# Optimization experiments

Hardware: AMD Instinct MI355X
Metric: run time of the kernel (lower is better)

Reference implementation:

```python
import jax, jax.numpy as jnp
import numpy as np

B, S, D, H, HD = 2, 4096, 768, 12, 64
W = 256          # one-sided window (attention_window=512)
G = 128          # number of global tokens (prefix)
NB = S // W      # sequence blocks
EPS = 1e-5


def _heads(x, w, b):
    # [B,S,D] -> [B,H,S,HD]
    return (x @ w + b).reshape(B, S, H, HD).transpose(0, 2, 1, 3)


def _blocks(xp):
    # xp: [B,H,S+2W,HD] (padded by W on both sides) -> [B,H,NB,3W,HD]
    # block n holds keys/values at absolute positions [n*W - W, n*W + 2W)
    return jnp.concatenate(
        [xp[:, :, j * W:j * W + S].reshape(B, H, NB, W, HD) for j in range(3)], axis=3)


def setup_inputs() -> dict:
    key = jax.random.key(0)
    ks = jax.random.split(key, 12)
    p = lambda i, shape: jax.random.normal(ks[i], shape, jnp.float32) * 0.02
    z = lambda n: jnp.zeros((n,), jnp.float32)
    return {
        'hidden_states': jax.random.normal(ks[0], (B, S, D), jnp.float32),
        'attention_mask': jnp.zeros((B, S), jnp.float32),  # 0 = local attention, no padding
        'is_index_global_attn': jnp.broadcast_to(jnp.arange(S) < G, (B, S)),
        'Wq': p(1, (D, D)), 'bq': z(D),
        'Wk': p(2, (D, D)), 'bk': z(D),
        'Wv': p(3, (D, D)), 'bv': z(D),
        'Wqg': p(4, (D, D)), 'bqg': z(D),
        'Wkg': p(5, (D, D)), 'bkg': z(D),
        'Wvg': p(6, (D, D)), 'bvg': z(D),
        'Wo': p(7, (D, D)), 'bo': z(D),
        'ln_gamma': jnp.ones((D,), jnp.float32),
        'ln_beta': jnp.zeros((D,), jnp.float32),
    }


def reference(hidden_states, attention_mask, is_index_global_attn,
              Wq, bq, Wk, bk, Wv, bv, Wqg, bqg, Wkg, bkg, Wvg, bvg,
              Wo, bo, ln_gamma, ln_beta):
    scale = 1.0 / np.sqrt(HD)
    q = _heads(hidden_states, Wq, bq) * scale   # [B,H,S,HD]
    k = _heads(hidden_states, Wk, bk)
    v = _heads(hidden_states, Wv, bv)

    pad = ((0, 0), (0, 0), (W, W), (0, 0))
    kb = _blocks(jnp.pad(k, pad))                # [B,H,NB,3W,HD]
    vb = _blocks(jnp.pad(v, pad))
    qb = q.reshape(B, H, NB, W, HD)
    s_band = jnp.einsum('bhnqd,bhnkd->bhnqk', qb, kb)   # [B,H,NB,W,3W]

    # band + boundary mask; global keys are removed from windowed attention
    # (they appear as dedicated prepended columns instead, as in HF Longformer)
    qi = jnp.arange(W)[:, None]                  # query offset in block
    kk = jnp.arange(3 * W)[None, :]              # key offset in 3W window
    rel = kk - W - qi                            # [W,3W] relative position
    kpos = jnp.arange(NB)[:, None, None] * W + (kk - W)[None]  # [NB,W(1),3W] absolute key pos
    valid = (jnp.abs(rel) <= W)[None] & (kpos >= G) & (kpos < S)  # [NB,W,3W]
    s_band = jnp.where(valid[None, None], s_band, -1e9)

    # global key columns (regular k/v projections, per HF Longformer)
    kg, vg = k[:, :, :G], v[:, :, :G]
    s_glob = jnp.einsum('bhsd,bhgd->bhsg', q, kg)        # [B,H,S,G]
    scores = jnp.concatenate([s_glob, s_band.reshape(B, H, S, 3 * W)], axis=-1)
    probs = jax.nn.softmax(scores, axis=-1)
    p_glob = probs[..., :G]
    p_band = probs[..., G:].reshape(B, H, NB, W, 3 * W)
    out = (jnp.einsum('bhnqk,bhnkd->bhnqd', p_band, vb).reshape(B, H, S, HD)
           + jnp.einsum('bhsg,bhgd->bhsd', p_glob, vg))

    # global query tokens attend to everything via the *_global projections;
    # their outputs overwrite the windowed outputs (HF behavior)
    qg = _heads(hidden_states, Wqg, bqg)[:, :, :G] * scale
    kgf = _heads(hidden_states, Wkg, bkg)
    vgf = _heads(hidden_states, Wvg, bvg)
    pg = jax.nn.softmax(jnp.einsum('bhgd,bhsd->bhgs', qg, kgf), axis=-1)
    og = jnp.einsum('bhgs,bhsd->bhgd', pg, vgf)
    out = out.at[:, :, :G].set(og)

    # TFLongformerSelfOutput: dense + residual + LayerNorm
    ctx = out.transpose(0, 2, 1, 3).reshape(B, S, D)
    y = ctx @ Wo + bo + hidden_states
    mu = y.mean(-1, keepdims=True)
    var = ((y - mu) ** 2).mean(-1, keepdims=True)
    return (y - mu) / jnp.sqrt(var + EPS) * ln_gamma + ln_beta
```

## Files before the change

kernel.cpp:

```cpp
#include <hip/hip_runtime.h>
#include <stdint.h>

#define BB 2
#define SS 4096
#define DD 768
#define HH 12
#define HDD 64
#define WW 256
#define GG 128
#define NBB 16
#define NSPLIT 16

typedef __attribute__((ext_vector_type(4))) float f32x4;
typedef __attribute__((ext_vector_type(16))) float f32x16;
typedef __attribute__((ext_vector_type(8))) short bf16x8;
typedef __attribute__((ext_vector_type(4))) short s16x4;
typedef __attribute__((ext_vector_type(4))) unsigned short u16x4;

__device__ __forceinline__ unsigned short f2bf(float x) {
  union { float f; unsigned int u; } v; v.f = x;
  return (unsigned short)((v.u + 0x7fffu + ((v.u >> 16) & 1u)) >> 16);
}

__device__ __forceinline__ void async16(void* lds, const void* g) {
  __builtin_amdgcn_global_load_lds(
      (const __attribute__((address_space(1))) unsigned int*)g,
      (__attribute__((address_space(3))) unsigned int*)lds, 16, 0, 0);
}

__device__ __forceinline__ uint32_t lds_b(const void* p) {
  return (uint32_t)(uintptr_t)(__attribute__((address_space(3))) const void*)p;
}

__device__ __forceinline__ s16x4 tr_read(uint32_t addr) {
  s16x4 d;
  asm volatile("ds_read_b64_tr_b16 %0, %1" : "=v"(d) : "v"(addr) : "memory");
  return d;
}

__device__ __forceinline__ unsigned int cvtpk(float lo, float hi) {
  unsigned int d;
  asm("v_cvt_pk_bf16_f32 %0, %1, %2" : "=v"(d) : "v"(lo), "v"(hi));
  return d;
}

__device__ __forceinline__ void plswap(int& a, int& b) {
  auto r = __builtin_amdgcn_permlane32_swap(a, b, false, false);
  a = r[0]; b = r[1];
}

__device__ __forceinline__ float xhalf(float x, int hi) {
  int a = __float_as_int(x), b = a;
  auto r = __builtin_amdgcn_permlane32_swap(a, b, false, false);
  return __int_as_float(hi ? r[0] : r[1]);
}

__global__ __launch_bounds__(256) void k_cvt(const float* __restrict__ x,
                                             unsigned short* __restrict__ o, int n4) {
  int i = blockIdx.x * 256 + threadIdx.x;
  if (i >= n4) return;
  f32x4 v = ((const f32x4*)x)[i];
  u16x4 r;
  r[0] = f2bf(v[0]); r[1] = f2bf(v[1]); r[2] = f2bf(v[2]); r[3] = f2bf(v[3]);
  ((u16x4*)o)[i] = r;
}

struct WArgs {
  const float* s[7];
  unsigned short* d[7];
};
__global__ __launch_bounds__(256) void k_tw(WArgs a) {
  __shared__ float t[64][65];
  const float* src = a.s[blockIdx.z];
  unsigned short* dst = a.d[blockIdx.z];
  int n0 = blockIdx.x * 64, k0 = blockIdx.y * 64;
#pragma unroll
  for (int it = 0; it < 16; ++it) {
    int idx = it * 256 + threadIdx.x;
    int r = idx >> 6, c = idx & 63;
    t[r][c] = src[(size_t)(k0 + r) * DD + n0 + c];
  }
  __syncthreads();
#pragma unroll
  for (int it = 0; it < 16; ++it) {
    int idx = it * 256 + threadIdx.x;
    int r = idx >> 6, c = idx & 63;
    dst[(size_t)(n0 + r) * DD + k0 + c] = f2bf(t[c][r]);
  }
}

template <int OMODE>
__global__ __launch_bounds__(256) void k_gemm(
    const unsigned short* __restrict__ A, const unsigned short* __restrict__ Wt,
    const float* __restrict__ b0, const float* __restrict__ b1,
    const float* __restrict__ b2, const float* __restrict__ b3,
    const float* __restrict__ b4, unsigned short* __restrict__ outH,
    float* __restrict__ outY, const float* __restrict__ resid) {
  const int bm = blockIdx.x;
  int bn, p;
  if (OMODE == 0) { p = blockIdx.y / 6; bn = blockIdx.y % 6; }
  else { p = 0; bn = blockIdx.y; }
  const float* bias = b0;
  if (OMODE == 0) bias = (p == 0) ? b0 : (p == 1) ? b1 : (p == 2) ? b2 : (p == 3) ? b3 : b4;
  const float scale = (OMODE == 1 || (OMODE == 0 && p == 0)) ? 0.125f : 1.0f;

  __shared__ unsigned short Asm_[128 * 64];
  __shared__ unsigned short Bsm_[128 * 64];
  const int tid = threadIdx.x;
  const int l = tid & 63, w = tid >> 6;
  const int wr = w >> 1, wc = w & 1;
  const int g = l >> 4, ln = l & 15;
  const int l3 = l >> 3, l7 = l & 7;
  const int slotsrc = l7 ^ l3;

  f32x4 zf = {0.f, 0.f, 0.f, 0.f};
  f32x4 acc[4][4];
#pragma unroll
  for (int i = 0; i < 4; ++i)
#pragma unroll
    for (int j = 0; j < 4; ++j) acc[i][j] = zf;

  const int wtrow0 = (OMODE == 0 ? p * DD : 0) + bn * 128;

  for (int kt = 0; kt < 12; ++kt) {
#pragma unroll
    for (int i = 0; i < 4; ++i) {
      int u = i * 4 + w;
      int row = u * 8 + l3;
      int ar = bm * 128 + row;
      if (OMODE == 1) ar = ((ar >> 7) << 12) + (ar & 127);
      async16(&Asm_[u * 512], A + (size_t)ar * DD + kt * 64 + slotsrc * 8);
      async16(&Bsm_[u * 512], Wt + (size_t)(wtrow0 + row) * DD + kt * 64 + slotsrc * 8);
    }
    __syncthreads();
#pragma unroll
    for (int kc = 0; kc < 2; ++kc) {
      bf16x8 af[4], bfr[4];
#pragma unroll
      for (int t = 0; t < 4; ++t) {
        int arow = wr * 64 + t * 16 + ln;
        af[t] = *(const bf16x8*)&Asm_[arow * 64 + (((kc * 4 + g) ^ (arow & 7)) << 3)];
        int brow = wc * 64 + t * 16 + ln;
        bfr[t] = *(const bf16x8*)&Bsm_[brow * 64 + (((kc * 4 + g) ^ (brow & 7)) << 3)];
      }
#pragma unroll
      for (int ti = 0; ti < 4; ++ti)
#pragma unroll
        for (int tj = 0; tj < 4; ++tj)
          acc[ti][tj] = __builtin_amdgcn_mfma_f32_16x16x32_bf16(af[ti], bfr[tj], acc[ti][tj], 0, 0, 0);
    }
    __syncthreads();
  }

#pragma unroll
  for (int tj = 0; tj < 4; ++tj) {
    int nl = bn * 128 + wc * 64 + tj * 16 + ln;
    float bv = bias[nl];
#pragma unroll
    for (int ti = 0; ti < 4; ++ti) {
#pragma unroll
      for (int r = 0; r < 4; ++r) {
        int m = bm * 128 + wr * 64 + ti * 16 + g * 4 + r;
        float val = acc[ti][tj][r] + bv;
        if (OMODE == 2) {
          outY[(size_t)m * DD + nl] = val + resid[(size_t)m * DD + nl];
        } else if (OMODE == 0) {
          val *= scale;
          int b = m >> 12, s = m & 4095, h = nl >> 6, d = nl & 63;
          outH[(size_t)p * (BB * HH * SS * HDD) +
               (((size_t)(b * HH + h) * SS + s) * HDD) + d] = f2bf(val);
        } else {
          val *= scale;
          int b = m >> 7, gi = m & 127, h = nl >> 6, d = nl & 63;
          outH[(((size_t)(b * HH + h) * GG + gi) * HDD) + d] = f2bf(val);
        }
      }
    }
  }
}

template <int MODE>
__global__ __launch_bounds__((MODE == 0) ? 512 : 256, 4) void k_attn(
    const unsigned short* __restrict__ qbuf, const unsigned short* __restrict__ kbuf,
    const unsigned short* __restrict__ vbuf, unsigned short* __restrict__ ctx,
    float* __restrict__ Opart, float* __restrict__ mlp) {
  constexpr int NW = (MODE == 0) ? 8 : 4;
  constexpr int NSTG = (MODE == 0) ? 1 : 2;
  constexpr float L2E = 1.4426950408889634f;

  __shared__ unsigned short Ksm[2][64 * 64];
  __shared__ unsigned short Vsm[2][64 * 64];
  __shared__ __align__(16) float Alds[NW][32];

  const int tid = threadIdx.x;
  const int l = tid & 63, w = tid >> 6;
  const int l31 = l & 31, hi = l >> 5;
  const int l3 = l >> 3, l7 = l & 7;

  int b, h, n, split;
  if (MODE == 0) {
    n = blockIdx.x & 15; h = (blockIdx.x >> 4) % 12; b = blockIdx.x / (16 * 12); split = 0;
  } else {
    split = blockIdx.x & 15; int bhid = blockIdx.x >> 4; h = bhid % 12; b = bhid / 12; n = 0;
  }

  const size_t bh = (size_t)(b * HH + h);
  const unsigned short* qp = qbuf + bh * (size_t)((MODE == 0) ? SS * HDD : GG * HDD);
  const unsigned short* kp = kbuf + bh * (size_t)(SS * HDD);
  const unsigned short* vp = vbuf + bh * (size_t)(SS * HDD);

  int bstart = 0, nch;
  if (MODE == 0) {
    bstart = n * 256 - 256;
    int s0 = bstart < GG ? GG : bstart;
    int e0 = bstart + 768; if (e0 > SS) e0 = SS;
    nch = 2 + ((e0 - s0) >> 6);
    bstart = s0;
  } else {
    nch = 4;
  }
  const int qrow0 = (MODE == 0) ? (n * 256 + w * 32) : (w * 32);

  bf16x8 qf[4];
#pragma unroll
  for (int kd = 0; kd < 4; ++kd)
    qf[kd] = *(const bf16x8*)&qp[(size_t)(qrow0 + l31) * HDD + kd * 16 + hi * 8];

  f32x16 O[2];
#pragma unroll
  for (int dt = 0; dt < 2; ++dt)
#pragma unroll
    for (int r = 0; r < 16; ++r) O[dt][r] = 0.f;
  float m2 = -1e30f, lsum = 0.f;

  const uint32_t vbase = lds_b(Vsm);
  int vwoff[NSTG];
  {
    int key0 = tid >> 3, dc = tid & 7;
#pragma unroll
    for (int u = 0; u < NSTG; ++u) {
      int key = u * 32 + key0;
      vwoff[u] = (((key >> 2) << 8) | ((dc >> 1) << 6) | ((key & 3) << 4) | ((dc & 1) << 3));
    }
  }

#define KB_OF(ci) ((ci) < 2 && MODE == 0 ? (ci) * 64 : (MODE == 0 ? bstart + ((ci) - 2) * 64 : ((split * 4 + (ci)) * 64)))

  bf16x8 vv[NSTG];
  {
    int kb = KB_OF(0);
#pragma unroll
    for (int u = 0; u < NSTG; ++u) {
      async16(&Ksm[0][(u * NW + w) * 512],
              kp + (size_t)(kb + (u * NW + w) * 8 + l3) * HDD + ((l7 ^ l3) << 3));
      vv[u] = *(const bf16x8*)&vp[(size_t)(kb + u * 32 + (tid >> 3)) * HDD + ((tid & 7) << 3)];
    }
  }
  int buf = 0;

  for (int ci = 0; ci < nch; ++ci) {
    const int kbase = KB_OF(ci);
    asm volatile("s_waitcnt vmcnt(0)" ::: "memory");
#pragma unroll
    for (int u = 0; u < NSTG; ++u) *(bf16x8*)&Vsm[buf][vwoff[u]] = vv[u];
    __syncthreads();

    if (ci + 1 < nch) {
      int kb = KB_OF(ci + 1);
#pragma unroll
      for (int u = 0; u < NSTG; ++u) {
        async16(&Ksm[buf ^ 1][(u * NW + w) * 512],
                kp + (size_t)(kb + (u * NW + w) * 8 + l3) * HDD + ((l7 ^ l3) << 3));
        vv[u] = *(const bf16x8*)&vp[(size_t)(kb + u * 32 + (tid >> 3)) * HDD + ((tid & 7) << 3)];
      }
    }

    f32x16 sc[2];
#pragma unroll
    for (int s = 0; s < 2; ++s)
#pragma unroll
      for (int r = 0; r < 16; ++r) sc[s][r] = 0.f;
    __builtin_amdgcn_s_setprio(1);
#pragma unroll
    for (int kd = 0; kd < 4; ++kd) {
#pragma unroll
      for (int s = 0; s < 2; ++s) {
        int row = s * 32 + l31;
        bf16x8 kf = *(const bf16x8*)&Ksm[buf][row * 64 + ((((kd << 1) + hi) ^ (row & 7)) << 3)];
        sc[s] = __builtin_amdgcn_mfma_f32_32x32x16_bf16(kf, qf[kd], sc[s], 0, 0, 0);
      }
    }
    __builtin_amdgcn_s_setprio(0);

    if (MODE == 0 && kbase >= GG) {
      const int base0 = (kbase - (n * 256 - 256)) - (w * 32 + l31);
#pragma unroll
      for (int s = 0; s < 2; ++s)
#pragma unroll
        for (int r = 0; r < 16; ++r) {
          int t = base0 + s * 32 + (r & 3) + 8 * (r >> 2) + 4 * hi;
          if ((unsigned)t > 512u) sc[s][r] = -1e9f;
        }
    }

    float mh = sc[0][0];
#pragma unroll
    for (int s = 0; s < 2; ++s)
#pragma unroll
      for (int r = 0; r < 16; ++r) if (s || r) mh = fmaxf(mh, sc[s][r]);
    mh = fmaxf(mh, xhalf(mh, hi));
    float mnew = fmaxf(m2, mh * L2E);
    float alpha = exp2f(m2 - mnew);
    m2 = mnew;
    float sh = 0.f;
#pragma unroll
    for (int s = 0; s < 2; ++s)
#pragma unroll
      for (int r = 0; r < 16; ++r) {
        float pv = exp2f(__builtin_fmaf(sc[s][r], L2E, -mnew));
        sc[s][r] = pv;
        sh += pv;
      }
    sh += xhalf(sh, hi);
    lsum = lsum * alpha + sh;

    if (l < 32) Alds[w][l] = alpha;
    f32x4 aT[4];
#pragma unroll
    for (int g2 = 0; g2 < 4; ++g2) aT[g2] = *(const f32x4*)&Alds[w][g2 * 8 + hi * 4];
#pragma unroll
    for (int dt = 0; dt < 2; ++dt)
#pragma unroll
      for (int r = 0; r < 16; ++r) O[dt][r] *= aT[r >> 2][r & 3];

    bf16x8 pa[4];
#pragma unroll
    for (int kk = 0; kk < 4; ++kk) {
      const int s = kk >> 1, h8 = (kk & 1) * 8;
      int x0 = (int)cvtpk(sc[s][h8 + 0], sc[s][h8 + 1]);
      int x1 = (int)cvtpk(sc[s][h8 + 2], sc[s][h8 + 3]);
      int y0 = (int)cvtpk(sc[s][h8 + 4], sc[s][h8 + 5]);
      int y1 = (int)cvtpk(sc[s][h8 + 6], sc[s][h8 + 7]);
      plswap(x0, y0); plswap(x1, y1);
      union { int u[4]; bf16x8 v; } pk;
      pk.u[0] = x0; pk.u[1] = x1; pk.u[2] = y0; pk.u[3] = y1;
      pa[kk] = pk.v;
    }

    const uint32_t vb = vbase + (uint32_t)(buf << 13);
#pragma unroll
    for (int dt = 0; dt < 2; ++dt) {
      s16x4 t0[4], t1[4];
#pragma unroll
      for (int kk = 0; kk < 4; ++kk) {
        int kg = kk * 4 + hi * 2;
        int dgrp = dt * 2 + (l31 >> 4);
        uint32_t a = vb + (uint32_t)((kg * 256 + dgrp * 64 + (l31 & 15)) << 1);
        t0[kk] = tr_read(a);
        t1[kk] = tr_read(a + 512);
      }
      asm volatile("s_waitcnt lgkmcnt(0)" ::: "memory");
      __builtin_amdgcn_sched_barrier(0);
      __builtin_amdgcn_s_setprio(1);
#pragma unroll
      for (int kk = 0; kk < 4; ++kk) {
        bf16x8 vf = __builtin_shufflevector(t0[kk], t1[kk], 0, 1, 2, 3, 4, 5, 6, 7);
        O[dt] = __builtin_amdgcn_mfma_f32_32x32x16_bf16(pa[kk], vf, O[dt], 0, 0, 0);
      }
      __builtin_amdgcn_s_setprio(0);
    }

    buf ^= 1;
  }

  if (MODE == 0) {
    if (l < 32) Alds[w][l] = 1.f / lsum;
    f32x4 iT[4];
#pragma unroll
    for (int g2 = 0; g2 < 4; ++g2) iT[g2] = *(const f32x4*)&Alds[w][g2 * 8 + hi * 4];
#pragma unroll
    for (int dt = 0; dt < 2; ++dt)
#pragma unroll
      for (int r = 0; r < 16; ++r) {
        int q = qrow0 + (r & 3) + 8 * (r >> 2) + 4 * hi;
        int d = dt * 32 + l31;
        ctx[((size_t)b * SS + q) * DD + h * HDD + d] = f2bf(O[dt][r] * iT[r >> 2][r & 3]);
      }
  } else {
    size_t pb = (bh * NSPLIT + split) * (size_t)GG;
#pragma unroll
    for (int dt = 0; dt < 2; ++dt)
#pragma unroll
      for (int r = 0; r < 16; ++r) {
        int q = w * 32 + (r & 3) + 8 * (r >> 2) + 4 * hi;
        Opart[(pb + q) * HDD + dt * 32 + l31] = O[dt][r];
      }
    if (l < 32) {
      size_t mb = (pb + w * 32 + l) * 2;
      mlp[mb] = m2;
      mlp[mb + 1] = lsum;
    }
  }
#undef KB_OF
}

__global__ __launch_bounds__(256) void k_red(const float* __restrict__ Opart,
                                             const float* __restrict__ mlp,
                                             unsigned short* __restrict__ ctx) {
  int wid = blockIdx.x * 4 + (threadIdx.x >> 6);
  int d = threadIdx.x & 63;
  int bh = wid >> 7, q = wid & 127;
  int b = bh / HH, h = bh % HH;

  float mmax = -1e30f;
#pragma unroll
  for (int s = 0; s < NSPLIT; ++s)
    mmax = fmaxf(mmax, mlp[(((size_t)bh * NSPLIT + s) * GG + q) * 2]);
  float acc = 0.f, denom = 0.f;
#pragma unroll
  for (int s = 0; s < NSPLIT; ++s) {
    size_t mb = (((size_t)bh * NSPLIT + s) * GG + q) * 2;
    float wgt = exp2f(mlp[mb] - mmax);
    denom += wgt * mlp[mb + 1];
    acc += wgt * Opart[(((size_t)bh * NSPLIT + s) * GG + q) * HDD + d];
  }
  ctx[((size_t)b * SS + q) * DD + h * HDD + d] = f2bf(acc / denom);
}

__global__ __launch_bounds__(256) void k_ln(const float* __restrict__ Y,
                                            const float* __restrict__ gam,
                                            const float* __restrict__ bet,
                                            float* __restrict__ outp) {
  const int row = blockIdx.x;
  const float* y = Y + (size_t)row * DD;
  float v0 = y[threadIdx.x], v1 = y[threadIdx.x + 256], v2 = y[threadIdx.x + 512];
  float s = v0 + v1 + v2, s2 = v0 * v0 + v1 * v1 + v2 * v2;
#pragma unroll
  for (int d = 1; d < 64; d <<= 1) { s += __shfl_xor(s, d, 64); s2 += __shfl_xor(s2, d, 64); }
  __shared__ float r1[4], r2[4];
  int w = threadIdx.x >> 6, l = threadIdx.x & 63;
  if (l == 0) { r1[w] = s; r2[w] = s2; }
  __syncthreads();
  s = r1[0] + r1[1] + r1[2] + r1[3];
  s2 = r2[0] + r2[1] + r2[2] + r2[3];
  float mu = s * (1.f / 768.f);
  float var = s2 * (1.f / 768.f) - mu * mu;
  float rstd = rsqrtf(var + 1e-5f);
  float* op = outp + (size_t)row * DD;
  op[threadIdx.x] = (v0 - mu) * rstd * gam[threadIdx.x] + bet[threadIdx.x];
  op[threadIdx.x + 256] = (v1 - mu) * rstd * gam[threadIdx.x + 256] + bet[threadIdx.x + 256];
  op[threadIdx.x + 512] = (v2 - mu) * rstd * gam[threadIdx.x + 512] + bet[threadIdx.x + 512];
}

extern "C" void kernel_launch(void* const* d_in, const int* in_sizes, int n_in,
                              void* d_out, int out_size, void* d_ws, size_t ws_size,
                              hipStream_t stream) {
  const float* hidden = (const float*)d_in[0];
  const float* Wq = (const float*)d_in[3];  const float* bq = (const float*)d_in[4];
  const float* Wk = (const float*)d_in[5];  const float* bk = (const float*)d_in[6];
  const float* Wv = (const float*)d_in[7];  const float* bv = (const float*)d_in[8];
  const float* Wqg = (const float*)d_in[9]; const float* bqg = (const float*)d_in[10];
  const float* Wkg = (const float*)d_in[11]; const float* bkg = (const float*)d_in[12];
  const float* Wvg = (const float*)d_in[13]; const float* bvg = (const float*)d_in[14];
  const float* Wo = (const float*)d_in[15]; const float* bo = (const float*)d_in[16];
  const float* gam = (const float*)d_in[17]; const float* bet = (const float*)d_in[18];

  char* ws = (char*)d_ws;
  const size_t SZH = (size_t)BB * HH * SS * HDD;
  unsigned short* xb = (unsigned short*)(ws);
  unsigned short* Wt5 = (unsigned short*)(ws + 12582912);
  unsigned short* Wtqg = (unsigned short*)(ws + 12582912 + 5898240);
  unsigned short* Wto = (unsigned short*)(ws + 12582912 + 5898240 + 1179648);
  unsigned short* qkv = (unsigned short*)(ws + 20840448);
  unsigned short* qg = (unsigned short*)(ws + 20840448 + 62914560);
  float* Opart = (float*)(ws + 84148224);
  float* mlp = (float*)(ws + 84148224 + 12582912);
  unsigned short* ctx = xb;
  float* Y = (float*)qkv;

  k_cvt<<<dim3((BB * SS * DD / 4 + 255) / 256), dim3(256), 0, stream>>>(hidden, xb, BB * SS * DD / 4);

  WArgs wa;
  wa.s[0] = Wq; wa.s[1] = Wk; wa.s[2] = Wv; wa.s[3] = Wkg; wa.s[4] = Wvg; wa.s[5] = Wqg; wa.s[6] = Wo;
  wa.d[0] = Wt5; wa.d[1] = Wt5 + 589824; wa.d[2] = Wt5 + 2 * 589824;
  wa.d[3] = Wt5 + 3 * 589824; wa.d[4] = Wt5 + 4 * 589824;
  wa.d[5] = Wtqg; wa.d[6] = Wto;
  k_tw<<<dim3(12, 12, 7), dim3(256), 0, stream>>>(wa);

  k_gemm<0><<<dim3(64, 30), dim3(256), 0, stream>>>(xb, Wt5, bq, bk, bv, bkg, bvg, qkv, nullptr, nullptr);
  k_gemm<1><<<dim3(2, 6), dim3(256), 0, stream>>>(xb, Wtqg, bqg, nullptr, nullptr, nullptr, nullptr, qg, nullptr, nullptr);

  k_attn<1><<<dim3(BB * HH * NSPLIT), dim3(256), 0, stream>>>(qg, qkv + 3 * SZH, qkv + 4 * SZH,
                                                              nullptr, Opart, mlp);
  k_attn<0><<<dim3(BB * HH * NBB), dim3(512), 0, stream>>>(qkv, qkv + SZH, qkv + 2 * SZH,
                                                           ctx, nullptr, nullptr);
  k_red<<<dim3(BB * HH * GG / 4), dim3(256), 0, stream>>>(Opart, mlp, ctx);

  k_gemm<2><<<dim3(64, 6), dim3(256), 0, stream>>>(ctx, Wto, bo, nullptr, nullptr, nullptr, nullptr, nullptr, Y, hidden);

  k_ln<<<dim3(BB * SS), dim3(256), 0, stream>>>(Y, gam, bet, (float*)d_out);
}
```

Before: 322.8 us.

## Add 256x256-tile double-buffered MFMA GEMM for fused QKV projection

Replaces the fused five-way projection GEMM with a new kernel that uses 256x256 output tiles, 512 threads, double-buffered async LDS staging with XOR swizzle, and a grouped workgroup-to-tile mapping for L2 locality. Larger tiles raise arithmetic intensity and cut redundant global loads of the activation and weight matrices. The cost is 128KB of LDS per workgroup and heavy register pressure from 32 accumulators per thread. Only 480 workgroups are launched, which may leave the device underfilled.

```diff
diff --git a/kernel.cpp b/kernel.cpp
--- a/kernel.cpp
+++ b/kernel.cpp
@@ -86,6 +86,116 @@
     int idx = it * 256 + threadIdx.x;
     int r = idx >> 6, c = idx & 63;
     dst[(size_t)(n0 + r) * DD + k0 + c] = f2bf(t[c][r]);
+  }
+}
+
+__device__ __forceinline__ void stage_tile(unsigned short* Abuf, unsigned short* Bbuf,
+                                           const unsigned short* ag,
+                                           const unsigned short* bg, int tid) {
+#pragma unroll
+  for (int u = 0; u < 4; ++u) {
+    async16(&Abuf[u * 4096 + tid * 8], ag + (size_t)u * 64 * DD);
+    async16(&Bbuf[u * 4096 + tid * 8], bg + (size_t)u * 64 * DD);
+  }
+}
+
+template <int OMODE>
+__global__ __launch_bounds__(512, 2) void k_gemm256(
+    const unsigned short* __restrict__ A, const unsigned short* __restrict__ Wt,
+    const float* __restrict__ b0, const float* __restrict__ b1,
+    const float* __restrict__ b2, const float* __restrict__ b3,
+    const float* __restrict__ b4, unsigned short* __restrict__ outH,
+    float* __restrict__ outY, const float* __restrict__ resid) {
+  constexpr int NCOL = (OMODE == 0) ? 15 : 3;
+  const int nwg = 32 * NCOL;
+  const int sw = (blockIdx.x & 7) * (nwg >> 3) + (blockIdx.x >> 3);
+  const int bx = sw & 31, by = sw >> 5;
+  const int M0 = bx * 256, N0 = by * 256;
+  const int p = (OMODE == 0) ? (by / 3) : 0;
+  const int N0p = N0 - p * DD;
+  const float* bias = b0;
+  if (OMODE == 0) bias = (p == 0) ? b0 : (p == 1) ? b1 : (p == 2) ? b2 : (p == 3) ? b3 : b4;
+  const float scale = (OMODE == 0 && p == 0) ? 0.125f : 1.0f;
+  const int WT0 = p * DD + N0p;
+
+  __shared__ unsigned short Al[2][256 * 64];
+  __shared__ unsigned short Bl[2][256 * 64];
+
+  const int tid = threadIdx.x;
+  const int l = tid & 63, w = tid >> 6;
+  const int wr = w >> 2, wc = w & 3;
+  const int g = l >> 4, ln = l & 15;
+  const int trow = tid >> 3;
+  const int tslot = (tid & 7) ^ (trow & 7);
+
+  f32x4 acc[8][4];
+#pragma unroll
+  for (int i = 0; i < 8; ++i)
+#pragma unroll
+    for (int j = 0; j < 4; ++j) acc[i][j] = (f32x4){0.f, 0.f, 0.f, 0.f};
+
+  const unsigned short* ag0 = A + (size_t)(M0 + trow) * DD + tslot * 8;
+  const unsigned short* bg0 = Wt + (size_t)(WT0 + trow) * DD + tslot * 8;
+
+  stage_tile(Al[0], Bl[0], ag0, bg0, tid);
+  stage_tile(Al[1], Bl[1], ag0 + 64, bg0 + 64, tid);
+
+  for (int kt = 0; kt < 12; ++kt) {
+    const int bb = kt & 1;
+    asm volatile("s_waitcnt vmcnt(8)" ::: "memory");
+    __builtin_amdgcn_s_barrier();
+
+    bf16x8 af[2][8], bfr[2][4];
+#pragma unroll
+    for (int kc = 0; kc < 2; ++kc) {
+#pragma unroll
+      for (int ti = 0; ti < 8; ++ti) {
+        int row = wr * 128 + ti * 16 + ln;
+        af[kc][ti] = *(const bf16x8*)&Al[bb][row * 64 + (((kc * 4 + g) ^ (row & 7)) << 3)];
+      }
+#pragma unroll
+      for (int tj = 0; tj < 4; ++tj) {
+        int row = wc * 64 + tj * 16 + ln;
+        bfr[kc][tj] = *(const bf16x8*)&Bl[bb][row * 64 + (((kc * 4 + g) ^ (row & 7)) << 3)];
+      }
+    }
+    __builtin_amdgcn_s_setprio(1);
+#pragma unroll
+    for (int kc = 0; kc < 2; ++kc)
+#pragma unroll
+      for (int ti = 0; ti < 8; ++ti)
+#pragma unroll
+        for (int tj = 0; tj < 4; ++tj)
+          acc[ti][tj] = __builtin_amdgcn_mfma_f32_16x16x32_bf16(af[kc][ti], bfr[kc][tj],
+                                                                acc[ti][tj], 0, 0, 0);
+    __builtin_amdgcn_s_setprio(0);
+    asm volatile("s_waitcnt lgkmcnt(0)" ::: "memory");
+    __builtin_amdgcn_sched_barrier(0);
+    __builtin_amdgcn_s_barrier();
+    if (kt + 2 < 12)
+      stage_tile(Al[bb], Bl[bb], ag0 + (kt + 2) * 64, bg0 + (kt + 2) * 64, tid);
+  }
+
+#pragma unroll
+  for (int tj = 0; tj < 4; ++tj) {
+    int npp = N0p + wc * 64 + tj * 16 + ln;
+    float bv = bias[npp];
+#pragma unroll
+    for (int ti = 0; ti < 8; ++ti) {
+#pragma unroll
+      for (int r2 = 0; r2 < 4; ++r2) {
+        int m = M0 + wr * 128 + ti * 16 + g * 4 + r2;
+        float val = acc[ti][tj][r2] + bv;
+        if (OMODE == 2) {
+          outY[(size_t)m * DD + npp] = val + resid[(size_t)m * DD + npp];
+        } else {
+          val *= scale;
+          int b = m >> 12, s = m & 4095, h = npp >> 6, d = npp & 63;
+          outH[(size_t)p * (BB * HH * SS * HDD) +
+               (((size_t)(b * HH + h) * SS + s) * HDD) + d] = f2bf(val);
+        }
+      }
+    }
   }
 }
 
@@ -487,7 +597,7 @@
   wa.d[5] = Wtqg; wa.d[6] = Wto;
   k_tw<<<dim3(12, 12, 7), dim3(256), 0, stream>>>(wa);
 
-  k_gemm<0><<<dim3(64, 30), dim3(256), 0, stream>>>(xb, Wt5, bq, bk, bv, bkg, bvg, qkv, nullptr, nullptr);
+  k_gemm256<0><<<dim3(480), dim3(512), 0, stream>>>(xb, Wt5, bq, bk, bv, bkg, bvg, qkv, nullptr, nullptr);
   k_gemm<1><<<dim3(2, 6), dim3(256), 0, stream>>>(xb, Wtqg, bqg, nullptr, nullptr, nullptr, nullptr, qg, nullptr, nullptr);
 
   k_attn<1><<<dim3(BB * HH * NSPLIT), dim3(256), 0, stream>>>(qg, qkv + 3 * SZH, qkv + 4 * SZH,
```

Result: no change. 321.5 us (-0.4%).
